# Kernel optimization log

Hardware: AMD Instinct MI355X
Metric: run time of the kernel (lower is better)

Reference implementation:

```python
import jax, jax.numpy as jnp
import numpy as np
import math

D_MODEL = 1024
NUM_HEADS = 16
HEAD_DIM = D_MODEL // NUM_HEADS


def _xavier(key, out_f, in_f):
    limit = math.sqrt(6.0 / (in_f + out_f))
    return jax.random.uniform(key, (out_f, in_f), jnp.float32, -limit, limit)


def ternarize(w):
    # abs-mean threshold -> {-1, 0, +1}
    abs_mean = jnp.mean(jnp.abs(w))
    return jnp.where(jnp.abs(w) > abs_mean, jnp.sign(w), jnp.zeros_like(w))


def setup_inputs() -> dict:
    key = jax.random.key(0)
    kq, kk, kv, kwq, kwk, kwv, kwo = jax.random.split(key, 7)
    B, S = 2, 2048
    return {
        "query": jax.random.normal(kq, (B, S, D_MODEL), jnp.float32),
        "key": jax.random.normal(kk, (B, S, D_MODEL), jnp.float32),
        "value": jax.random.normal(kv, (B, S, D_MODEL), jnp.float32),
        "w_q": _xavier(kwq, D_MODEL, D_MODEL),
        "w_k": _xavier(kwk, D_MODEL, D_MODEL),
        "w_v": _xavier(kwv, D_MODEL, D_MODEL),
        "w_o": _xavier(kwo, D_MODEL, D_MODEL),
    }


def reference(query, key, value, w_q, w_k, w_v, w_o):
    B, S, _ = query.shape
    # ternary projections (F.linear: x @ W.T)
    q = query @ ternarize(w_q).T
    k = key @ ternarize(w_k).T
    v = value @ ternarize(w_v).T
    # [B, H, S, Dh]
    q = q.reshape(B, S, NUM_HEADS, HEAD_DIM).transpose(0, 2, 1, 3)
    k = k.reshape(B, -1, NUM_HEADS, HEAD_DIM).transpose(0, 2, 1, 3)
    v = v.reshape(B, -1, NUM_HEADS, HEAD_DIM).transpose(0, 2, 1, 3)
    scores = jnp.einsum("bhqd,bhkd->bhqk", q, k) / math.sqrt(HEAD_DIM)
    probs = jax.nn.softmax(scores, axis=-1)
    out = jnp.einsum("bhqk,bhkd->bhqd", probs, v)
    out = out.transpose(0, 2, 1, 3).reshape(B, S, D_MODEL)
    return out @ ternarize(w_o).T
```

## Files before the change

### kernel.cpp

```cpp
#include <hip/hip_runtime.h>
#include <cstdint>
#include <cstddef>

typedef __bf16 bfloat;
typedef __bf16 bf16x8 __attribute__((ext_vector_type(8)));
typedef __bf16 bf16x4 __attribute__((ext_vector_type(4)));
typedef float  f32x4  __attribute__((ext_vector_type(4)));

static constexpr int D  = 1024;
static constexpr int S  = 2048;
static constexpr int B  = 2;
static constexpr int H  = 16;
static constexpr int DH = 64;
static constexpr int M  = B * S;
static constexpr int WMAT_N = 1024 * 1024;

#define MFMA_BF16(a, b, c) __builtin_amdgcn_mfma_f32_16x16x32_bf16((a), (b), (c), 0, 0, 0)

__device__ __forceinline__ void gl_lds16(const void* g, void* l) {
  __builtin_amdgcn_global_load_lds(
      (const __attribute__((address_space(1))) void*)g,
      (__attribute__((address_space(3))) void*)l, 16, 0, 0);
}

__global__ void absum_kernel(const float* __restrict__ w0, const float* __restrict__ w1,
                             const float* __restrict__ w2, const float* __restrict__ w3,
                             double* __restrict__ sums) {
  int z = blockIdx.y;
  const float* w = (z == 0) ? w0 : (z == 1) ? w1 : (z == 2) ? w2 : w3;
  const float4* w4 = (const float4*)w;
  double s = 0.0;
  for (int i = blockIdx.x * blockDim.x + threadIdx.x; i < (WMAT_N / 4);
       i += gridDim.x * blockDim.x) {
    float4 v = w4[i];
    s += (double)fabsf(v.x) + (double)fabsf(v.y) + (double)fabsf(v.z) + (double)fabsf(v.w);
  }
  for (int off = 1; off < 64; off <<= 1) s += __shfl_xor(s, off, 64);
  __shared__ double ps[4];
  if ((threadIdx.x & 63) == 0) ps[threadIdx.x >> 6] = s;
  __syncthreads();
  if (threadIdx.x == 0) atomicAdd(&sums[z], ps[0] + ps[1] + ps[2] + ps[3]);
}

__global__ void tern_kernel(const float* __restrict__ w0, const float* __restrict__ w1,
                            const float* __restrict__ w2, const float* __restrict__ w3,
                            bfloat* __restrict__ o0, bfloat* __restrict__ o1,
                            bfloat* __restrict__ o2, bfloat* __restrict__ o3,
                            const double* __restrict__ sums) {
  int z = blockIdx.y;
  const float* w = (z == 0) ? w0 : (z == 1) ? w1 : (z == 2) ? w2 : w3;
  bfloat* o = (z == 0) ? o0 : (z == 1) ? o1 : (z == 2) ? o2 : o3;
  double thr = sums[z] * (1.0 / (double)WMAT_N);
  const float4* w4 = (const float4*)w;
  for (int i = blockIdx.x * blockDim.x + threadIdx.x; i < (WMAT_N / 4);
       i += gridDim.x * blockDim.x) {
    float4 v = w4[i];
    bf16x4 r;
    r[0] = (bfloat)(((double)fabsf(v.x) > thr) ? (v.x > 0.f ? 1.f : -1.f) : 0.f);
    r[1] = (bfloat)(((double)fabsf(v.y) > thr) ? (v.y > 0.f ? 1.f : -1.f) : 0.f);
    r[2] = (bfloat)(((double)fabsf(v.z) > thr) ? (v.z > 0.f ? 1.f : -1.f) : 0.f);
    r[3] = (bfloat)(((double)fabsf(v.w) > thr) ? (v.w > 0.f ? 1.f : -1.f) : 0.f);
    *(bf16x4*)&o[(size_t)i * 4] = r;
  }
}

__global__ void splitcvt3_kernel(const float* __restrict__ qx, const float* __restrict__ kx,
                                 const float* __restrict__ vx, bfloat* __restrict__ qhi,
                                 bfloat* __restrict__ qlo, bfloat* __restrict__ khi,
                                 bfloat* __restrict__ klo, bfloat* __restrict__ vhi) {
  int z = blockIdx.y;
  const float* x = (z == 0) ? qx : (z == 1) ? kx : vx;
  bfloat* hi = (z == 0) ? qhi : (z == 1) ? khi : vhi;
  bfloat* lo = (z == 0) ? qlo : (z == 1) ? klo : nullptr;
  const int n4 = M * D / 4;
  const float4* x4 = (const float4*)x;
  for (int i = blockIdx.x * blockDim.x + threadIdx.x; i < n4; i += gridDim.x * blockDim.x) {
    float4 v = x4[i];
    bf16x4 h;
    h[0] = (bfloat)v.x; h[1] = (bfloat)v.y; h[2] = (bfloat)v.z; h[3] = (bfloat)v.w;
    *(bf16x4*)&hi[(size_t)i * 4] = h;
    if (z < 2) {
      bf16x4 l;
      l[0] = (bfloat)(v.x - (float)h[0]);
      l[1] = (bfloat)(v.y - (float)h[1]);
      l[2] = (bfloat)(v.z - (float)h[2]);
      l[3] = (bfloat)(v.w - (float)h[3]);
      *(bf16x4*)&lo[(size_t)i * 4] = l;
    }
  }
}

__global__ __launch_bounds__(256) void qkv_gemm(
    const bfloat* __restrict__ xqh, const bfloat* __restrict__ xql,
    const bfloat* __restrict__ xkh, const bfloat* __restrict__ xkl,
    const bfloat* __restrict__ xvh, const bfloat* __restrict__ wqt,
    const bfloat* __restrict__ wkt, const bfloat* __restrict__ wvt,
    bfloat* __restrict__ qmh, bfloat* __restrict__ qml,
    bfloat* __restrict__ kmh, bfloat* __restrict__ kml, bfloat* __restrict__ vtr) {
  constexpr int K = D;
  constexpr int N = D;
  __shared__ __align__(16) bfloat As0[128 * 32];
  __shared__ __align__(16) bfloat As1[128 * 32];
  __shared__ __align__(16) bfloat Ws[128 * 32];

  const int z = blockIdx.z;
  const bfloat *A0, *A1 = nullptr, *Wm;
  bfloat *Oh = nullptr, *Ol = nullptr;
  float scale = 1.f;
  bool split;
  if (z == 0) {
    A0 = xqh; A1 = xql; Wm = wqt; Oh = qmh; Ol = qml;
    scale = 0.18033688f;
    split = true;
  } else if (z == 1) {
    A0 = xkh; A1 = xkl; Wm = wkt; Oh = kmh; Ol = kml; split = true;
  } else {
    A0 = xvh; Wm = wvt; split = false;
  }

  const int t = threadIdx.x;
  const int w = t >> 6, lane = t & 63;
  const int quad = lane >> 4, l16 = lane & 15;
  const int wm = w >> 1, wn = w & 1;
  const int m0 = blockIdx.y * 128, n0 = blockIdx.x * 128;

  f32x4 acc[4][4] = {};

  const int sr = t >> 2;
  const int sc = (t & 3) * 8;

  const bfloat* pA0a = A0 + (size_t)(m0 + sr) * K + sc;
  const bfloat* pA0b = A0 + (size_t)(m0 + 64 + sr) * K + sc;
  const bfloat* pA1a = split ? A1 + (size_t)(m0 + sr) * K + sc : nullptr;
  const bfloat* pA1b = split ? A1 + (size_t)(m0 + 64 + sr) * K + sc : nullptr;
  const bfloat* pWa = Wm + (size_t)(n0 + sr) * K + sc;
  const bfloat* pWb = Wm + (size_t)(n0 + 64 + sr) * K + sc;

  for (int kk = 0; kk < K; kk += 32) {
    gl_lds16(pA0a + kk, As0 + w * 512);
    gl_lds16(pA0b + kk, As0 + 2048 + w * 512);
    if (split) {
      gl_lds16(pA1a + kk, As1 + w * 512);
      gl_lds16(pA1b + kk, As1 + 2048 + w * 512);
    }
    gl_lds16(pWa + kk, Ws + w * 512);
    gl_lds16(pWb + kk, Ws + 2048 + w * 512);
    __syncthreads();

    bf16x8 bfrag[4], afrag[4];
#pragma unroll
    for (int nt = 0; nt < 4; nt++)
      bfrag[nt] = *(const bf16x8*)&Ws[(wn * 64 + nt * 16 + l16) * 32 + quad * 8];
#pragma unroll
    for (int mt = 0; mt < 4; mt++)
      afrag[mt] = *(const bf16x8*)&As0[(wm * 64 + mt * 16 + l16) * 32 + quad * 8];
#pragma unroll
    for (int mt = 0; mt < 4; mt++)
#pragma unroll
      for (int nt = 0; nt < 4; nt++)
        acc[mt][nt] = MFMA_BF16(afrag[mt], bfrag[nt], acc[mt][nt]);
    if (split) {
#pragma unroll
      for (int mt = 0; mt < 4; mt++)
        afrag[mt] = *(const bf16x8*)&As1[(wm * 64 + mt * 16 + l16) * 32 + quad * 8];
#pragma unroll
      for (int mt = 0; mt < 4; mt++)
#pragma unroll
        for (int nt = 0; nt < 4; nt++)
          acc[mt][nt] = MFMA_BF16(afrag[mt], bfrag[nt], acc[mt][nt]);
    }
    __syncthreads();
  }

#pragma unroll
  for (int mt = 0; mt < 4; mt++) {
#pragma unroll
    for (int nt = 0; nt < 4; nt++) {
      const int row = m0 + wm * 64 + mt * 16 + quad * 4;
      const int col = n0 + wn * 64 + nt * 16 + l16;
      if (split) {
#pragma unroll
        for (int rg = 0; rg < 4; rg++) {
          float vv = acc[mt][nt][rg] * scale;
          size_t idx = (size_t)(row + rg) * N + col;
          bfloat hh = (bfloat)vv;
          Oh[idx] = hh;
          Ol[idx] = (bfloat)(vv - (float)hh);
        }
      } else {
        int bb = row >> 11, s = row & (S - 1);
        bf16x4 pk;
#pragma unroll
        for (int rg = 0; rg < 4; rg++) pk[rg] = (bfloat)acc[mt][nt][rg];
        *(bf16x4*)&vtr[(size_t)bb * D * S + (size_t)col * S + s] = pk;
      }
    }
  }
}

__global__ __launch_bounds__(256) void gemm_wo(const bfloat* __restrict__ A,
                                               const bfloat* __restrict__ Wm,
                                               float* __restrict__ Cf) {
  constexpr int K = D;
  constexpr int N = D;
  __shared__ __align__(16) bfloat As[128 * 32];
  __shared__ __align__(16) bfloat Ws[64 * 32];

  const int t = threadIdx.x;
  const int w = t >> 6, lane = t & 63;
  const int quad = lane >> 4, l16 = lane & 15;
  const int wm = w >> 1, wn = w & 1;
  const int m0 = blockIdx.y * 128, n0 = blockIdx.x * 64;

  f32x4 acc[4][2] = {};

  const int sr = t >> 2;
  const int sc = (t & 3) * 8;
  const bfloat* pAa = A + (size_t)(m0 + sr) * K + sc;
  const bfloat* pAb = A + (size_t)(m0 + 64 + sr) * K + sc;
  const bfloat* pW = Wm + (size_t)(n0 + sr) * K + sc;

  for (int kk = 0; kk < K; kk += 32) {
    gl_lds16(pAa + kk, As + w * 512);
    gl_lds16(pAb + kk, As + 2048 + w * 512);
    gl_lds16(pW + kk, Ws + w * 512);
    __syncthreads();

    bf16x8 bfrag[2], afrag[4];
#pragma unroll
    for (int nt = 0; nt < 2; nt++)
      bfrag[nt] = *(const bf16x8*)&Ws[(wn * 32 + nt * 16 + l16) * 32 + quad * 8];
#pragma unroll
    for (int mt = 0; mt < 4; mt++)
      afrag[mt] = *(const bf16x8*)&As[(wm * 64 + mt * 16 + l16) * 32 + quad * 8];
#pragma unroll
    for (int mt = 0; mt < 4; mt++)
#pragma unroll
      for (int nt = 0; nt < 2; nt++)
        acc[mt][nt] = MFMA_BF16(afrag[mt], bfrag[nt], acc[mt][nt]);
    __syncthreads();
  }

#pragma unroll
  for (int mt = 0; mt < 4; mt++) {
#pragma unroll
    for (int nt = 0; nt < 2; nt++) {
      const int row = m0 + wm * 64 + mt * 16 + quad * 4;
      const int col = n0 + wn * 32 + nt * 16 + l16;
#pragma unroll
      for (int rg = 0; rg < 4; rg++) Cf[(size_t)(row + rg) * N + col] = acc[mt][nt][rg];
    }
  }
}

__global__ __launch_bounds__(256) void flash_kernel(
    const bfloat* __restrict__ qh, const bfloat* __restrict__ ql,
    const bfloat* __restrict__ kh, const bfloat* __restrict__ kl,
    const bfloat* __restrict__ vt, bfloat* __restrict__ outp) {
  __shared__ __align__(16) bfloat Kh[64 * 64];
  __shared__ __align__(16) bfloat Kl[64 * 64];
  __shared__ __align__(16) bfloat Vt[64 * 64];
  __shared__ __align__(16) bfloat Pm[64 * 64];

  const int t = threadIdx.x;
  const int w = t >> 6, lane = t & 63;
  const int quad = lane >> 4, l16 = lane & 15;
  const int b = blockIdx.z, h = blockIdx.y;
  const int q0 = blockIdx.x * 64;
  const size_t base = (size_t)b * S * D + (size_t)h * DH;
  const size_t vbase = (size_t)b * D * S + (size_t)h * DH * S;

  const int ssr = lane >> 3;
  const int spc = lane & 7;

  bf16x8 ones;
#pragma unroll
  for (int j = 0; j < 8; j++) ones[j] = (bfloat)1.f;

#pragma unroll
  for (int g = 0; g < 2; g++) {
    int r = w * 16 + g * 8 + ssr;
    int c = spc ^ (r & 7);
    int lo = (w * 16 + g * 8) * 64;
    gl_lds16(qh + base + (size_t)(q0 + r) * D + c * 8, Kh + lo);
    gl_lds16(ql + base + (size_t)(q0 + r) * D + c * 8, Kl + lo);
  }
  __syncthreads();
  bf16x8 qhf[2], qlf[2];
  {
    int row = w * 16 + l16;
#pragma unroll
    for (int s2 = 0; s2 < 2; s2++) {
      qhf[s2] = *(const bf16x8*)&Kh[row * 64 + (((s2 * 4 + quad) ^ (l16 & 7)) * 8)];
      qlf[s2] = *(const bf16x8*)&Kl[row * 64 + (((s2 * 4 + quad) ^ (l16 & 7)) * 8)];
    }
  }
  __syncthreads();

  f32x4 Oa[4] = {};
  f32x4 La = {};
  float m_i = -3.0e38f;

  for (int k0 = 0; k0 < S; k0 += 64) {
#pragma unroll
    for (int g = 0; g < 2; g++) {
      int r = w * 16 + g * 8 + ssr;
      int c = spc ^ (r & 7);
      int lo = (w * 16 + g * 8) * 64;
      gl_lds16(kh + base + (size_t)(k0 + r) * D + c * 8, Kh + lo);
      gl_lds16(kl + base + (size_t)(k0 + r) * D + c * 8, Kl + lo);
      gl_lds16(vt + vbase + (size_t)r * S + k0 + c * 8, Vt + lo);
    }
    __syncthreads();

    f32x4 sf[4];
#pragma unroll
    for (int mt = 0; mt < 4; mt++) {
      f32x4 a = {};
      int krow = mt * 16 + l16;
#pragma unroll
      for (int s2 = 0; s2 < 2; s2++) {
        bf16x8 bh = *(const bf16x8*)&Kh[krow * 64 + (((s2 * 4 + quad) ^ (l16 & 7)) * 8)];
        bf16x8 bl = *(const bf16x8*)&Kl[krow * 64 + (((s2 * 4 + quad) ^ (l16 & 7)) * 8)];
        a = MFMA_BF16(bh, qhf[s2], a);
        a = MFMA_BF16(bl, qhf[s2], a);
        a = MFMA_BF16(bh, qlf[s2], a);
      }
      sf[mt] = a;
    }

    float mm = sf[0][0];
#pragma unroll
    for (int mt = 0; mt < 4; mt++)
#pragma unroll
      for (int rg = 0; rg < 4; rg++) mm = fmaxf(mm, sf[mt][rg]);
    mm = fmaxf(mm, __shfl_xor(mm, 16, 64));
    mm = fmaxf(mm, __shfl_xor(mm, 32, 64));
    float mnew = fmaxf(m_i, mm);
    float alpha = exp2f(m_i - mnew);
    m_i = mnew;
#pragma unroll
    for (int mt = 0; mt < 4; mt++)
#pragma unroll
      for (int rg = 0; rg < 4; rg++) sf[mt][rg] = exp2f(sf[mt][rg] - mnew);
#pragma unroll
    for (int mt = 0; mt < 4; mt++) Oa[mt] *= alpha;
    La *= alpha;

#pragma unroll
    for (int mt = 0; mt < 4; mt++) {
      bf16x4 pk;
#pragma unroll
      for (int rg = 0; rg < 4; rg++) pk[rg] = (bfloat)sf[mt][rg];
      int g16 = (mt * 2 + (quad >> 1)) ^ (l16 & 7);
      *(bf16x4*)&Pm[(w * 16 + l16) * 64 + g16 * 8 + (quad & 1) * 4] = pk;
    }

#pragma unroll
    for (int s2 = 0; s2 < 2; s2++) {
      bf16x8 pb = *(const bf16x8*)&Pm[(w * 16 + l16) * 64 +
                                      (((s2 * 4 + quad) ^ (l16 & 7)) * 8)];
#pragma unroll
      for (int mt = 0; mt < 4; mt++) {
        int vrow = mt * 16 + l16;
        bf16x8 va = *(const bf16x8*)&Vt[vrow * 64 + (((s2 * 4 + quad) ^ (l16 & 7)) * 8)];
        Oa[mt] = MFMA_BF16(va, pb, Oa[mt]);
      }
      La = MFMA_BF16(ones, pb, La);
    }
    __syncthreads();
  }

  float inv = 1.0f / La[0];
  const int qrow = q0 + w * 16 + l16;
#pragma unroll
  for (int mt = 0; mt < 4; mt++) {
    bf16x4 ov;
#pragma unroll
    for (int rg = 0; rg < 4; rg++) ov[rg] = (bfloat)(Oa[mt][rg] * inv);
    *(bf16x4*)&outp[base + (size_t)qrow * D + mt * 16 + quad * 4] = ov;
  }
}

extern "C" void kernel_launch(void* const* d_in, const int* in_sizes, int n_in,
                              void* d_out, int out_size, void* d_ws, size_t ws_size,
                              hipStream_t stream) {
  const float* q_in = (const float*)d_in[0];
  const float* k_in = (const float*)d_in[1];
  const float* v_in = (const float*)d_in[2];
  const float* wq = (const float*)d_in[3];
  const float* wk = (const float*)d_in[4];
  const float* wv = (const float*)d_in[5];
  const float* wo = (const float*)d_in[6];
  float* outp = (float*)d_out;
  char* ws = (char*)d_ws;

  constexpr size_t WBYTES = (size_t)WMAT_N * 2;
  constexpr size_t XBYTES = (size_t)M * D * 2;
  size_t off = 0;
  double* sums = (double*)(ws + off); off += 256;
  bfloat* wqt = (bfloat*)(ws + off); off += WBYTES;
  bfloat* wkt = (bfloat*)(ws + off); off += WBYTES;
  bfloat* wvt = (bfloat*)(ws + off); off += WBYTES;
  bfloat* wot = (bfloat*)(ws + off); off += WBYTES;
  bfloat* xqh = (bfloat*)(ws + off); off += XBYTES;
  bfloat* xql = (bfloat*)(ws + off); off += XBYTES;
  bfloat* xkh = (bfloat*)(ws + off); off += XBYTES;
  bfloat* xkl = (bfloat*)(ws + off); off += XBYTES;
  bfloat* xvh = (bfloat*)(ws + off); off += XBYTES;
  bfloat* qmh = (bfloat*)(ws + off); off += XBYTES;
  bfloat* qml = (bfloat*)(ws + off); off += XBYTES;
  bfloat* kmh = (bfloat*)(ws + off); off += XBYTES;
  bfloat* kml = (bfloat*)(ws + off); off += XBYTES;
  bfloat* vtr = (bfloat*)(ws + off); off += XBYTES;
  bfloat* attn = xqh;

  hipMemsetAsync(sums, 0, 4 * sizeof(double), stream);
  absum_kernel<<<dim3(128, 4), 256, 0, stream>>>(wq, wk, wv, wo, sums);
  tern_kernel<<<dim3(128, 4), 256, 0, stream>>>(wq, wk, wv, wo, wqt, wkt, wvt, wot, sums);
  splitcvt3_kernel<<<dim3(512, 3), 256, 0, stream>>>(q_in, k_in, v_in, xqh, xql, xkh, xkl, xvh);
  qkv_gemm<<<dim3(D / 128, M / 128, 3), 256, 0, stream>>>(
      xqh, xql, xkh, xkl, xvh, wqt, wkt, wvt, qmh, qml, kmh, kml, vtr);
  flash_kernel<<<dim3(S / 64, H, B), 256, 0, stream>>>(qmh, qml, kmh, kml, vtr, attn);
  gemm_wo<<<dim3(D / 64, M / 128), 256, 0, stream>>>(attn, wot, outp);
}
```

Measured before the change: 301.9 us.

## Fuse fp32-to-bf16 hi/lo split into QKV GEMM and widen K tiles with swizzle

Removes the separate split-convert kernel. The QKV GEMM now loads fp32 activations straight into swizzled LDS and converts them to bf16 hi/lo fragments in registers, which avoids writing and re-reading five bf16 activation copies. Both GEMMs move to a 64-wide K tile with an XOR-swizzled LDS layout, halving the number of barriers. The flash kernel skips the running-max rescale when no lane's max increases. The cost is more LDS per block (fp32 tile), in-register conversion work repeated by every N-tile block, and possibly lower occupancy.

```diff
diff --git a/kernel.cpp b/kernel.cpp
--- a/kernel.cpp
+++ b/kernel.cpp
@@ -64,59 +64,25 @@
   }
 }
 
-__global__ void splitcvt3_kernel(const float* __restrict__ qx, const float* __restrict__ kx,
-                                 const float* __restrict__ vx, bfloat* __restrict__ qhi,
-                                 bfloat* __restrict__ qlo, bfloat* __restrict__ khi,
-                                 bfloat* __restrict__ klo, bfloat* __restrict__ vhi) {
-  int z = blockIdx.y;
-  const float* x = (z == 0) ? qx : (z == 1) ? kx : vx;
-  bfloat* hi = (z == 0) ? qhi : (z == 1) ? khi : vhi;
-  bfloat* lo = (z == 0) ? qlo : (z == 1) ? klo : nullptr;
-  const int n4 = M * D / 4;
-  const float4* x4 = (const float4*)x;
-  for (int i = blockIdx.x * blockDim.x + threadIdx.x; i < n4; i += gridDim.x * blockDim.x) {
-    float4 v = x4[i];
-    bf16x4 h;
-    h[0] = (bfloat)v.x; h[1] = (bfloat)v.y; h[2] = (bfloat)v.z; h[3] = (bfloat)v.w;
-    *(bf16x4*)&hi[(size_t)i * 4] = h;
-    if (z < 2) {
-      bf16x4 l;
-      l[0] = (bfloat)(v.x - (float)h[0]);
-      l[1] = (bfloat)(v.y - (float)h[1]);
-      l[2] = (bfloat)(v.z - (float)h[2]);
-      l[3] = (bfloat)(v.w - (float)h[3]);
-      *(bf16x4*)&lo[(size_t)i * 4] = l;
-    }
-  }
-}
-
 __global__ __launch_bounds__(256) void qkv_gemm(
-    const bfloat* __restrict__ xqh, const bfloat* __restrict__ xql,
-    const bfloat* __restrict__ xkh, const bfloat* __restrict__ xkl,
-    const bfloat* __restrict__ xvh, const bfloat* __restrict__ wqt,
+    const float* __restrict__ xq, const float* __restrict__ xk,
+    const float* __restrict__ xv, const bfloat* __restrict__ wqt,
     const bfloat* __restrict__ wkt, const bfloat* __restrict__ wvt,
     bfloat* __restrict__ qmh, bfloat* __restrict__ qml,
-    bfloat* __restrict__ kmh, bfloat* __restrict__ kml, bfloat* __restrict__ vtr) {
+    bfloat* __restrict__ kmh, bfloat* __restrict__ kml,
+    bfloat* __restrict__ vtr) {
   constexpr int K = D;
   constexpr int N = D;
-  __shared__ __align__(16) bfloat As0[128 * 32];
-  __shared__ __align__(16) bfloat As1[128 * 32];
-  __shared__ __align__(16) bfloat Ws[128 * 32];
+  __shared__ __align__(16) float  Xs[128 * 64];
+  __shared__ __align__(16) bfloat Ws[128 * 64];
 
   const int z = blockIdx.z;
-  const bfloat *A0, *A1 = nullptr, *Wm;
-  bfloat *Oh = nullptr, *Ol = nullptr;
-  float scale = 1.f;
-  bool split;
-  if (z == 0) {
-    A0 = xqh; A1 = xql; Wm = wqt; Oh = qmh; Ol = qml;
-    scale = 0.18033688f;
-    split = true;
-  } else if (z == 1) {
-    A0 = xkh; A1 = xkl; Wm = wkt; Oh = kmh; Ol = kml; split = true;
-  } else {
-    A0 = xvh; Wm = wvt; split = false;
-  }
+  const float* A = (z == 0) ? xq : (z == 1) ? xk : xv;
+  const bfloat* Wm = (z == 0) ? wqt : (z == 1) ? wkt : wvt;
+  bfloat* Oh = (z == 0) ? qmh : kmh;
+  bfloat* Ol = (z == 0) ? qml : kml;
+  const bool split = (z < 2);
+  const float scale = (z == 0) ? 0.18033688f : 1.f;
 
   const int t = threadIdx.x;
   const int w = t >> 6, lane = t & 63;
@@ -126,48 +92,62 @@
 
   f32x4 acc[4][4] = {};
 
-  const int sr = t >> 2;
-  const int sc = (t & 3) * 8;
-
-  const bfloat* pA0a = A0 + (size_t)(m0 + sr) * K + sc;
-  const bfloat* pA0b = A0 + (size_t)(m0 + 64 + sr) * K + sc;
-  const bfloat* pA1a = split ? A1 + (size_t)(m0 + sr) * K + sc : nullptr;
-  const bfloat* pA1b = split ? A1 + (size_t)(m0 + 64 + sr) * K + sc : nullptr;
-  const bfloat* pWa = Wm + (size_t)(n0 + sr) * K + sc;
-  const bfloat* pWb = Wm + (size_t)(n0 + 64 + sr) * K + sc;
-
-  for (int kk = 0; kk < K; kk += 32) {
-    gl_lds16(pA0a + kk, As0 + w * 512);
-    gl_lds16(pA0b + kk, As0 + 2048 + w * 512);
-    if (split) {
-      gl_lds16(pA1a + kk, As1 + w * 512);
-      gl_lds16(pA1b + kk, As1 + 2048 + w * 512);
-    }
-    gl_lds16(pWa + kk, Ws + w * 512);
-    gl_lds16(pWb + kk, Ws + 2048 + w * 512);
-    __syncthreads();
-
-    bf16x8 bfrag[4], afrag[4];
-#pragma unroll
-    for (int nt = 0; nt < 4; nt++)
-      bfrag[nt] = *(const bf16x8*)&Ws[(wn * 64 + nt * 16 + l16) * 32 + quad * 8];
-#pragma unroll
-    for (int mt = 0; mt < 4; mt++)
-      afrag[mt] = *(const bf16x8*)&As0[(wm * 64 + mt * 16 + l16) * 32 + quad * 8];
-#pragma unroll
-    for (int mt = 0; mt < 4; mt++)
-#pragma unroll
-      for (int nt = 0; nt < 4; nt++)
-        acc[mt][nt] = MFMA_BF16(afrag[mt], bfrag[nt], acc[mt][nt]);
-    if (split) {
+  const int r4 = lane >> 4, cp16 = lane & 15;
+  const int r8 = lane >> 3, cp8 = lane & 7;
+
+  for (int kk = 0; kk < K; kk += 64) {
+#pragma unroll
+    for (int g = 0; g < 8; g++) {
+      int row = w * 32 + g * 4 + r4;
+      int cl = cp16 ^ (row & 15);
+      gl_lds16(A + (size_t)(m0 + row) * K + kk + cl * 4, Xs + (w * 32 + g * 4) * 64);
+    }
+#pragma unroll
+    for (int g = 0; g < 4; g++) {
+      int row = w * 32 + g * 8 + r8;
+      int cl = cp8 ^ (row & 7);
+      gl_lds16(Wm + (size_t)(n0 + row) * K + kk + cl * 8, Ws + (w * 32 + g * 8) * 64);
+    }
+    __syncthreads();
+
+#pragma unroll
+    for (int kidx = 0; kidx < 2; kidx++) {
+      bf16x8 bfrag[4], ah[4], al[4];
+#pragma unroll
+      for (int nt = 0; nt < 4; nt++) {
+        int row = wn * 64 + nt * 16 + l16;
+        bfrag[nt] =
+            *(const bf16x8*)&Ws[row * 64 + (((kidx * 4 + quad) ^ (l16 & 7)) * 8)];
+      }
+#pragma unroll
+      for (int mt = 0; mt < 4; mt++) {
+        int row = wm * 64 + mt * 16 + l16;
+        int cl0 = kidx * 8 + quad * 2;
+        f32x4 fa = *(const f32x4*)&Xs[row * 64 + ((cl0 ^ l16) * 4)];
+        f32x4 fb = *(const f32x4*)&Xs[row * 64 + (((cl0 + 1) ^ l16) * 4)];
+#pragma unroll
+        for (int j = 0; j < 4; j++) {
+          bfloat h0 = (bfloat)fa[j], h1 = (bfloat)fb[j];
+          ah[mt][j] = h0;
+          ah[mt][j + 4] = h1;
+          if (split) {
+            al[mt][j] = (bfloat)(fa[j] - (float)h0);
+            al[mt][j + 4] = (bfloat)(fb[j] - (float)h1);
+          }
+        }
+      }
 #pragma unroll
       for (int mt = 0; mt < 4; mt++)
-        afrag[mt] = *(const bf16x8*)&As1[(wm * 64 + mt * 16 + l16) * 32 + quad * 8];
-#pragma unroll
-      for (int mt = 0; mt < 4; mt++)
 #pragma unroll
         for (int nt = 0; nt < 4; nt++)
-          acc[mt][nt] = MFMA_BF16(afrag[mt], bfrag[nt], acc[mt][nt]);
+          acc[mt][nt] = MFMA_BF16(ah[mt], bfrag[nt], acc[mt][nt]);
+      if (split) {
+#pragma unroll
+        for (int mt = 0; mt < 4; mt++)
+#pragma unroll
+          for (int nt = 0; nt < 4; nt++)
+            acc[mt][nt] = MFMA_BF16(al[mt], bfrag[nt], acc[mt][nt]);
+      }
     }
     __syncthreads();
   }
@@ -203,8 +183,8 @@
                                                float* __restrict__ Cf) {
   constexpr int K = D;
   constexpr int N = D;
-  __shared__ __align__(16) bfloat As[128 * 32];
-  __shared__ __align__(16) bfloat Ws[64 * 32];
+  __shared__ __align__(16) bfloat As[128 * 64];
+  __shared__ __align__(16) bfloat Ws[64 * 64];
 
   const int t = threadIdx.x;
   const int w = t >> 6, lane = t & 63;
@@ -214,30 +194,44 @@
 
   f32x4 acc[4][2] = {};
 
-  const int sr = t >> 2;
-  const int sc = (t & 3) * 8;
-  const bfloat* pAa = A + (size_t)(m0 + sr) * K + sc;
-  const bfloat* pAb = A + (size_t)(m0 + 64 + sr) * K + sc;
-  const bfloat* pW = Wm + (size_t)(n0 + sr) * K + sc;
-
-  for (int kk = 0; kk < K; kk += 32) {
-    gl_lds16(pAa + kk, As + w * 512);
-    gl_lds16(pAb + kk, As + 2048 + w * 512);
-    gl_lds16(pW + kk, Ws + w * 512);
-    __syncthreads();
-
-    bf16x8 bfrag[2], afrag[4];
-#pragma unroll
-    for (int nt = 0; nt < 2; nt++)
-      bfrag[nt] = *(const bf16x8*)&Ws[(wn * 32 + nt * 16 + l16) * 32 + quad * 8];
-#pragma unroll
-    for (int mt = 0; mt < 4; mt++)
-      afrag[mt] = *(const bf16x8*)&As[(wm * 64 + mt * 16 + l16) * 32 + quad * 8];
-#pragma unroll
-    for (int mt = 0; mt < 4; mt++)
-#pragma unroll
-      for (int nt = 0; nt < 2; nt++)
-        acc[mt][nt] = MFMA_BF16(afrag[mt], bfrag[nt], acc[mt][nt]);
+  const int r8 = lane >> 3, cp8 = lane & 7;
+
+  for (int kk = 0; kk < K; kk += 64) {
+#pragma unroll
+    for (int g = 0; g < 4; g++) {
+      int row = w * 32 + g * 8 + r8;
+      int cl = cp8 ^ (row & 7);
+      gl_lds16(A + (size_t)(m0 + row) * K + kk + cl * 8, As + (w * 32 + g * 8) * 64);
+    }
+#pragma unroll
+    for (int g = 0; g < 2; g++) {
+      int row = w * 16 + g * 8 + r8;
+      int cl = cp8 ^ (row & 7);
+      gl_lds16(Wm + (size_t)(n0 + row) * K + kk + cl * 8, Ws + (w * 16 + g * 8) * 64);
+    }
+    __syncthreads();
+
+#pragma unroll
+    for (int kidx = 0; kidx < 2; kidx++) {
+      bf16x8 bfrag[2], afrag[4];
+#pragma unroll
+      for (int nt = 0; nt < 2; nt++) {
+        int row = wn * 32 + nt * 16 + l16;
+        bfrag[nt] =
+            *(const bf16x8*)&Ws[row * 64 + (((kidx * 4 + quad) ^ (l16 & 7)) * 8)];
+      }
+#pragma unroll
+      for (int mt = 0; mt < 4; mt++) {
+        int row = wm * 64 + mt * 16 + l16;
+        afrag[mt] =
+            *(const bf16x8*)&As[row * 64 + (((kidx * 4 + quad) ^ (l16 & 7)) * 8)];
+      }
+#pragma unroll
+      for (int mt = 0; mt < 4; mt++)
+#pragma unroll
+        for (int nt = 0; nt < 2; nt++)
+          acc[mt][nt] = MFMA_BF16(afrag[mt], bfrag[nt], acc[mt][nt]);
+    }
     __syncthreads();
   }
 
@@ -336,16 +330,18 @@
       for (int rg = 0; rg < 4; rg++) mm = fmaxf(mm, sf[mt][rg]);
     mm = fmaxf(mm, __shfl_xor(mm, 16, 64));
     mm = fmaxf(mm, __shfl_xor(mm, 32, 64));
-    float mnew = fmaxf(m_i, mm);
-    float alpha = exp2f(m_i - mnew);
-    m_i = mnew;
+    if (__ballot(mm > m_i)) {
+      float mnew = fmaxf(m_i, mm);
+      float alpha = exp2f(m_i - mnew);
+      m_i = mnew;
+#pragma unroll
+      for (int mt = 0; mt < 4; mt++) Oa[mt] *= alpha;
+      La *= alpha;
+    }
 #pragma unroll
     for (int mt = 0; mt < 4; mt++)
 #pragma unroll
-      for (int rg = 0; rg < 4; rg++) sf[mt][rg] = exp2f(sf[mt][rg] - mnew);
-#pragma unroll
-    for (int mt = 0; mt < 4; mt++) Oa[mt] *= alpha;
-    La *= alpha;
+      for (int rg = 0; rg < 4; rg++) sf[mt][rg] = exp2f(sf[mt][rg] - m_i);
 
 #pragma unroll
     for (int mt = 0; mt < 4; mt++) {
@@ -403,24 +399,18 @@
   bfloat* wkt = (bfloat*)(ws + off); off += WBYTES;
   bfloat* wvt = (bfloat*)(ws + off); off += WBYTES;
   bfloat* wot = (bfloat*)(ws + off); off += WBYTES;
-  bfloat* xqh = (bfloat*)(ws + off); off += XBYTES;
-  bfloat* xql = (bfloat*)(ws + off); off += XBYTES;
-  bfloat* xkh = (bfloat*)(ws + off); off += XBYTES;
-  bfloat* xkl = (bfloat*)(ws + off); off += XBYTES;
-  bfloat* xvh = (bfloat*)(ws + off); off += XBYTES;
   bfloat* qmh = (bfloat*)(ws + off); off += XBYTES;
   bfloat* qml = (bfloat*)(ws + off); off += XBYTES;
   bfloat* kmh = (bfloat*)(ws + off); off += XBYTES;
   bfloat* kml = (bfloat*)(ws + off); off += XBYTES;
   bfloat* vtr = (bfloat*)(ws + off); off += XBYTES;
-  bfloat* attn = xqh;
+  bfloat* attn = (bfloat*)(ws + off); off += XBYTES;
 
   hipMemsetAsync(sums, 0, 4 * sizeof(double), stream);
   absum_kernel<<<dim3(128, 4), 256, 0, stream>>>(wq, wk, wv, wo, sums);
   tern_kernel<<<dim3(128, 4), 256, 0, stream>>>(wq, wk, wv, wo, wqt, wkt, wvt, wot, sums);
-  splitcvt3_kernel<<<dim3(512, 3), 256, 0, stream>>>(q_in, k_in, v_in, xqh, xql, xkh, xkl, xvh);
   qkv_gemm<<<dim3(D / 128, M / 128, 3), 256, 0, stream>>>(
-      xqh, xql, xkh, xkl, xvh, wqt, wkt, wvt, qmh, qml, kmh, kml, vtr);
+      q_in, k_in, v_in, wqt, wkt, wvt, qmh, qml, kmh, kml, vtr);
   flash_kernel<<<dim3(S / 64, H, B), 256, 0, stream>>>(qmh, qml, kmh, kml, vtr, attn);
   gemm_wo<<<dim3(D / 64, M / 128), 256, 0, stream>>>(attn, wot, outp);
 }
```

Result: slower. 313.6 us (+3.9%).

## Swizzle GEMM LDS tiles and skip softmax rescale when max unchanged

Applied to the files above, without the earlier changes.

Applies an XOR swizzle to the 16-byte chunk column in the LDS tiles of both projection GEMMs. The global-to-LDS loads fetch permuted columns and the fragment reads undo the permutation, which is meant to reduce LDS bank conflicts on the bf16x8 fragment loads. In the attention kernel, the online-softmax rescale of the output accumulators and row sum now runs only when some lane's running max increases, using a wave-uniform ballot. This saves exp and multiply work on most later key blocks at the cost of a branch.

```diff
diff --git a/kernel.cpp b/kernel.cpp
--- a/kernel.cpp
+++ b/kernel.cpp
@@ -127,14 +127,16 @@
   f32x4 acc[4][4] = {};
 
   const int sr = t >> 2;
-  const int sc = (t & 3) * 8;
-
-  const bfloat* pA0a = A0 + (size_t)(m0 + sr) * K + sc;
-  const bfloat* pA0b = A0 + (size_t)(m0 + 64 + sr) * K + sc;
-  const bfloat* pA1a = split ? A1 + (size_t)(m0 + sr) * K + sc : nullptr;
-  const bfloat* pA1b = split ? A1 + (size_t)(m0 + 64 + sr) * K + sc : nullptr;
-  const bfloat* pWa = Wm + (size_t)(n0 + sr) * K + sc;
-  const bfloat* pWb = Wm + (size_t)(n0 + 64 + sr) * K + sc;
+  const int cp = t & 3;
+  const int cla = cp ^ ((sr >> 1) & 3);
+  const int clb = cp ^ (((sr + 64) >> 1) & 3);
+
+  const bfloat* pA0a = A0 + (size_t)(m0 + sr) * K + cla * 8;
+  const bfloat* pA0b = A0 + (size_t)(m0 + 64 + sr) * K + clb * 8;
+  const bfloat* pA1a = split ? A1 + (size_t)(m0 + sr) * K + cla * 8 : nullptr;
+  const bfloat* pA1b = split ? A1 + (size_t)(m0 + 64 + sr) * K + clb * 8 : nullptr;
+  const bfloat* pWa = Wm + (size_t)(n0 + sr) * K + cla * 8;
+  const bfloat* pWb = Wm + (size_t)(n0 + 64 + sr) * K + clb * 8;
 
   for (int kk = 0; kk < K; kk += 32) {
     gl_lds16(pA0a + kk, As0 + w * 512);
@@ -149,11 +151,15 @@
 
     bf16x8 bfrag[4], afrag[4];
 #pragma unroll
-    for (int nt = 0; nt < 4; nt++)
-      bfrag[nt] = *(const bf16x8*)&Ws[(wn * 64 + nt * 16 + l16) * 32 + quad * 8];
-#pragma unroll
-    for (int mt = 0; mt < 4; mt++)
-      afrag[mt] = *(const bf16x8*)&As0[(wm * 64 + mt * 16 + l16) * 32 + quad * 8];
+    for (int nt = 0; nt < 4; nt++) {
+      int r = wn * 64 + nt * 16 + l16;
+      bfrag[nt] = *(const bf16x8*)&Ws[r * 32 + ((quad ^ ((r >> 1) & 3)) * 8)];
+    }
+#pragma unroll
+    for (int mt = 0; mt < 4; mt++) {
+      int r = wm * 64 + mt * 16 + l16;
+      afrag[mt] = *(const bf16x8*)&As0[r * 32 + ((quad ^ ((r >> 1) & 3)) * 8)];
+    }
 #pragma unroll
     for (int mt = 0; mt < 4; mt++)
 #pragma unroll
@@ -161,8 +167,10 @@
         acc[mt][nt] = MFMA_BF16(afrag[mt], bfrag[nt], acc[mt][nt]);
     if (split) {
 #pragma unroll
-      for (int mt = 0; mt < 4; mt++)
-        afrag[mt] = *(const bf16x8*)&As1[(wm * 64 + mt * 16 + l16) * 32 + quad * 8];
+      for (int mt = 0; mt < 4; mt++) {
+        int r = wm * 64 + mt * 16 + l16;
+        afrag[mt] = *(const bf16x8*)&As1[r * 32 + ((quad ^ ((r >> 1) & 3)) * 8)];
+      }
 #pragma unroll
       for (int mt = 0; mt < 4; mt++)
 #pragma unroll
@@ -215,10 +223,12 @@
   f32x4 acc[4][2] = {};
 
   const int sr = t >> 2;
-  const int sc = (t & 3) * 8;
-  const bfloat* pAa = A + (size_t)(m0 + sr) * K + sc;
-  const bfloat* pAb = A + (size_t)(m0 + 64 + sr) * K + sc;
-  const bfloat* pW = Wm + (size_t)(n0 + sr) * K + sc;
+  const int cp = t & 3;
+  const int cla = cp ^ ((sr >> 1) & 3);
+  const int clb = cp ^ (((sr + 64) >> 1) & 3);
+  const bfloat* pAa = A + (size_t)(m0 + sr) * K + cla * 8;
+  const bfloat* pAb = A + (size_t)(m0 + 64 + sr) * K + clb * 8;
+  const bfloat* pW = Wm + (size_t)(n0 + sr) * K + cla * 8;
 
   for (int kk = 0; kk < K; kk += 32) {
     gl_lds16(pAa + kk, As + w * 512);
@@ -228,11 +238,15 @@
 
     bf16x8 bfrag[2], afrag[4];
 #pragma unroll
-    for (int nt = 0; nt < 2; nt++)
-      bfrag[nt] = *(const bf16x8*)&Ws[(wn * 32 + nt * 16 + l16) * 32 + quad * 8];
-#pragma unroll
-    for (int mt = 0; mt < 4; mt++)
-      afrag[mt] = *(const bf16x8*)&As[(wm * 64 + mt * 16 + l16) * 32 + quad * 8];
+    for (int nt = 0; nt < 2; nt++) {
+      int r = wn * 32 + nt * 16 + l16;
+      bfrag[nt] = *(const bf16x8*)&Ws[r * 32 + ((quad ^ ((r >> 1) & 3)) * 8)];
+    }
+#pragma unroll
+    for (int mt = 0; mt < 4; mt++) {
+      int r = wm * 64 + mt * 16 + l16;
+      afrag[mt] = *(const bf16x8*)&As[r * 32 + ((quad ^ ((r >> 1) & 3)) * 8)];
+    }
 #pragma unroll
     for (int mt = 0; mt < 4; mt++)
 #pragma unroll
@@ -336,16 +350,18 @@
       for (int rg = 0; rg < 4; rg++) mm = fmaxf(mm, sf[mt][rg]);
     mm = fmaxf(mm, __shfl_xor(mm, 16, 64));
     mm = fmaxf(mm, __shfl_xor(mm, 32, 64));
-    float mnew = fmaxf(m_i, mm);
-    float alpha = exp2f(m_i - mnew);
-    m_i = mnew;
+    if (__ballot(mm > m_i)) {
+      float mnew = fmaxf(m_i, mm);
+      float alpha = exp2f(m_i - mnew);
+      m_i = mnew;
+#pragma unroll
+      for (int mt = 0; mt < 4; mt++) Oa[mt] *= alpha;
+      La *= alpha;
+    }
 #pragma unroll
     for (int mt = 0; mt < 4; mt++)
 #pragma unroll
-      for (int rg = 0; rg < 4; rg++) sf[mt][rg] = exp2f(sf[mt][rg] - mnew);
-#pragma unroll
-    for (int mt = 0; mt < 4; mt++) Oa[mt] *= alpha;
-    La *= alpha;
+      for (int rg = 0; rg < 4; rg++) sf[mt][rg] = exp2f(sf[mt][rg] - m_i);
 
 #pragma unroll
     for (int mt = 0; mt < 4; mt++) {
```

Measured after the change: 299.4 us. No clear change (-0.8%).
